# Optimization experiments

Hardware: AMD Instinct MI355X
Metric: run time of the kernel (lower is better)

## Reference

```python
import jax, jax.numpy as jnp
import numpy as np

NEG_SLOPE = 0.2  # PyG GATConv default leaky_relu slope
EPS = 1e-16


def setup_inputs() -> dict:
    key = jax.random.key(0)
    ks = jax.random.split(key, 8)
    N, E, F = 50000, 1600000, 128
    L, H, C = 3, 4, 32  # layers, heads, per-head channels; H*C == F
    Dh = 32             # MLP hidden (== hidden_channels)
    x = jax.random.normal(ks[0], (N, F), jnp.float32)
    edge_index = jax.random.randint(ks[1], (2, E), 0, N, jnp.int32)
    W = jax.random.normal(ks[2], (L, F, H * C), jnp.float32) * 0.1
    att_src = jax.random.normal(ks[3], (L, H, C), jnp.float32) * 0.1
    att_dst = jax.random.normal(ks[4], (L, H, C), jnp.float32) * 0.1
    b_conv = jnp.zeros((L, H * C), jnp.float32)
    W1 = jax.random.normal(ks[5], (F + H * C, Dh), jnp.float32) * 0.1
    b1 = jnp.zeros((Dh,), jnp.float32)
    W2 = jax.random.normal(ks[6], (Dh, 1), jnp.float32) * 0.1
    b2 = jnp.zeros((1,), jnp.float32)
    return {"x": x, "edge_index": edge_index, "W": W, "att_src": att_src,
            "att_dst": att_dst, "b_conv": b_conv, "W1": W1, "b1": b1,
            "W2": W2, "b2": b2}


def _gat_layer(x, src, dst, W, a_s, a_d, b, N):
    H, C = a_s.shape
    h = (x @ W).reshape(N, H, C)                      # [N,H,C]
    alpha_s = jnp.sum(h * a_s, axis=-1)               # [N,H]
    alpha_d = jnp.sum(h * a_d, axis=-1)               # [N,H]
    e = jax.nn.leaky_relu(alpha_s[src] + alpha_d[dst], NEG_SLOPE)  # [E,H]
    # segment softmax over incoming edges of each dst node
    m = jax.ops.segment_max(e, dst, num_segments=N)
    ex = jnp.exp(e - m[dst])
    s = jax.ops.segment_sum(ex, dst, num_segments=N)
    a = ex / (s[dst] + EPS)                           # [E,H]
    out = jax.ops.segment_sum(h[src] * a[:, :, None], dst, num_segments=N)
    return out.reshape(N, H * C) + b


def reference(x, edge_index, W, att_src, att_dst, b_conv, W1, b1, W2, b2):
    N = x.shape[0]
    loops = jnp.arange(N, dtype=edge_index.dtype)
    src = jnp.concatenate([edge_index[0], loops])  # PyG GATConv adds self loops
    dst = jnp.concatenate([edge_index[1], loops])
    x0 = x
    for l in range(W.shape[0]):
        x = _gat_layer(x, src, dst, W[l], att_src[l], att_dst[l], b_conv[l], N)
    h = jnp.concatenate([x, x0], axis=-1)
    h = jax.nn.relu(h @ W1 + b1)
    return jax.nn.sigmoid(h @ W2 + b2)
```

## Files before the change

### kernel.cpp

```cpp
#include <hip/hip_runtime.h>

#define NEG_SLOPE 0.2f
#define EPSF 1e-16f

typedef unsigned int uint;
typedef unsigned short ushort;
typedef __attribute__((ext_vector_type(8))) short short8;
typedef __attribute__((ext_vector_type(4))) float floatx4;

static __device__ __forceinline__ ushort f2bf(float f) {
    uint u = __float_as_uint(f);
    return (ushort)((u + 0x7FFFu + ((u >> 16) & 1u)) >> 16);
}
static __device__ __forceinline__ uint pack2(float a, float b) {
    return (uint)f2bf(a) | ((uint)f2bf(b) << 16);
}
static __device__ __forceinline__ float bf_lo(uint p) { return __uint_as_float(p << 16); }
static __device__ __forceinline__ float bf_hi(uint p) { return __uint_as_float(p & 0xFFFF0000u); }
static __device__ __forceinline__ short8 u2s8(uint4 v) {
    union { uint4 u; short8 s; } c; c.u = v; return c.s;
}
static __device__ __forceinline__ void load_lds16(const void* g, void* l) {
    __builtin_amdgcn_global_load_lds(
        (const __attribute__((address_space(1))) void*)g,
        (__attribute__((address_space(3))) void*)l, 16, 0, 0);
}

__global__ __launch_bounds__(256) void prep_kernel(
    const float* __restrict__ W, const float* __restrict__ W1,
    const float* __restrict__ x, uint4* __restrict__ Wp,
    uint4* __restrict__ W1p, uint4* __restrict__ xb,
    int* __restrict__ bucket_count, int L, int N)
{
    int id = blockIdx.x * 256 + threadIdx.x;
    const int nW = L * 2048;
    const int nX = N * 16;
    if (id < nW) {
        int l = id >> 11, s = id & 2047;
        int chunk = s >> 7, col = s & 127;
        const float* wp = W + (size_t)l * 16384 + (chunk * 8) * 128 + col;
        uint4 pk;
        pk.x = pack2(wp[0],   wp[128]);
        pk.y = pack2(wp[256], wp[384]);
        pk.z = pack2(wp[512], wp[640]);
        pk.w = pack2(wp[768], wp[896]);
        Wp[id] = pk;
    } else if (id < nW + 1024) {
        int s = id - nW;
        int chunk = s >> 5, col = s & 31;
        const float* wp = W1 + (chunk * 8) * 32 + col;
        uint4 pk;
        pk.x = pack2(wp[0],   wp[32]);
        pk.y = pack2(wp[64],  wp[96]);
        pk.z = pack2(wp[128], wp[160]);
        pk.w = pack2(wp[192], wp[224]);
        W1p[s] = pk;
    } else if (id < nW + 1024 + nX) {
        int xid = id - nW - 1024;
        int row = xid >> 4, c8 = xid & 15;
        const float4* xp = (const float4*)(x + (size_t)row * 128 + c8 * 8);
        float4 v0 = xp[0], v1 = xp[1];
        uint4 pk;
        pk.x = pack2(v0.x, v0.y); pk.y = pack2(v0.z, v0.w);
        pk.z = pack2(v1.x, v1.y); pk.w = pack2(v1.z, v1.w);
        xb[xid] = pk;
    } else if (id < nW + 1024 + nX + 256) {
        bucket_count[id - nW - 1024 - nX] = 0;
    }
}

#define GA_LDS_BYTES ((2048 + 1040) * 16)
__global__ __launch_bounds__(256) void gemm_alpha_kernel(
    const uint4* __restrict__ xb, const uint4* __restrict__ Wp,
    const float* __restrict__ att_s, const float* __restrict__ att_d,
    uint* __restrict__ h2, float* __restrict__ alpha_s,
    float* __restrict__ alpha_d, int N)
{
    __shared__ __align__(16) char smraw[GA_LDS_BYTES];
    uint4* sW = (uint4*)smraw;
    uint4* sX = sW + 2048;
    float* sD = (float*)smraw;

    const int t = threadIdx.x;
    const int wb = t & ~63;
    const int rowBase = blockIdx.x * 64;

#pragma unroll
    for (int i = 0; i < 8; ++i)
        load_lds16(Wp + i * 256 + t, sW + i * 256 + wb);

#pragma unroll
    for (int i = 0; i < 4; ++i) {
        int f = t + i * 256;
        int row = f >> 4, c8 = f & 15;
        uint4 v = make_uint4(0u, 0u, 0u, 0u);
        if (rowBase + row < N) v = xb[(size_t)(rowBase + row) * 16 + c8];
        sX[c8 * 65 + row] = v;
    }
    __syncthreads();

    const int w = t >> 6, lane = t & 63, q = lane >> 4, l15 = lane & 15;
    short8 a[4];
#pragma unroll
    for (int s = 0; s < 4; ++s)
        a[s] = u2s8(sX[(4 * s + q) * 65 + 16 * w + l15]);

    floatx4 acc[8];
#pragma unroll
    for (int ct = 0; ct < 8; ++ct) acc[ct] = (floatx4){0.f, 0.f, 0.f, 0.f};
#pragma unroll
    for (int ct = 0; ct < 8; ++ct) {
#pragma unroll
        for (int s = 0; s < 4; ++s) {
            short8 b = u2s8(sW[(4 * s + q) * 128 + 16 * ct + l15]);
            acc[ct] = __builtin_amdgcn_mfma_f32_16x16x32_bf16(a[s], b, acc[ct], 0, 0, 0);
        }
    }
    __syncthreads();

#pragma unroll
    for (int ct = 0; ct < 8; ++ct) {
#pragma unroll
        for (int r = 0; r < 4; ++r)
            sD[(16 * w + 4 * q + r) * 129 + 16 * ct + l15] = acc[ct][r];
    }
    __syncthreads();

#pragma unroll
    for (int i = 0; i < 4; ++i) {
        int slot = t + i * 256;
        int row = slot >> 4, c8 = slot & 15;
        if (rowBase + row < N) {
            const float* dp = &sD[row * 129 + c8 * 8];
            uint4 o;
            o.x = pack2(dp[0], dp[1]); o.y = pack2(dp[2], dp[3]);
            o.z = pack2(dp[4], dp[5]); o.w = pack2(dp[6], dp[7]);
            ((uint4*)h2)[(size_t)(rowBase + row) * 16 + c8] = o;
        }
    }
    {
        int row = t & 63, head = t >> 6;
        if (rowBase + row < N) {
            const float* dp = &sD[row * 129 + head * 32];
            const float* asp = att_s + head * 32;
            const float* adp = att_d + head * 32;
            float ps = 0.f, pd = 0.f;
#pragma unroll
            for (int c = 0; c < 32; ++c) { float v = dp[c]; ps += v * asp[c]; pd += v * adp[c]; }
            alpha_s[(size_t)(rowBase + row) * 4 + head] = ps;
            alpha_d[(size_t)(rowBase + row) * 4 + head] = pd;
        }
    }
}

__global__ __launch_bounds__(256) void bucket_count_kernel(
    const int* __restrict__ ei, int E, int NB, int* __restrict__ bucket_count)
{
    __shared__ int cnt[256];
    cnt[threadIdx.x] = 0;
    __syncthreads();
    const int base = blockIdx.x * 2048 + threadIdx.x;
#pragma unroll
    for (int j = 0; j < 8; ++j) {
        int idx = base + j * 256;
        if (idx < E) atomicAdd(&cnt[ei[E + idx] >> 8], 1);
    }
    __syncthreads();
    int c = cnt[threadIdx.x];
    if (threadIdx.x < NB && c) atomicAdd(&bucket_count[threadIdx.x], c);
}

__global__ __launch_bounds__(256) void bucket_scan_kernel(
    const int* __restrict__ bucket_count, int NB,
    int* __restrict__ bucket_base, int* __restrict__ bucket_cursor,
    int* __restrict__ row_start, int N)
{
    __shared__ int s[256];
    const int t = threadIdx.x;
    int v = (t < NB) ? bucket_count[t] : 0;
    s[t] = v;
    __syncthreads();
    for (int off = 1; off < 256; off <<= 1) {
        int x = s[t];
        int a = (t >= off) ? s[t - off] : 0;
        __syncthreads();
        s[t] = x + a;
        __syncthreads();
    }
    int ex = s[t] - v;
    if (t < NB) { bucket_base[t] = ex; bucket_cursor[t] = ex; }
    if (t == 255) { bucket_base[NB] = s[255]; row_start[N] = s[255]; }
}

__global__ __launch_bounds__(256) void distribute_kernel(
    const int* __restrict__ ei, int E, int NB,
    int* __restrict__ bucket_cursor, uint* __restrict__ bdata)
{
    __shared__ int cnt[256];
    __shared__ int bbase[256];
    cnt[threadIdx.x] = 0;
    __syncthreads();
    const int base = blockIdx.x * 2048 + threadIdx.x;
    int srcs[8], dsts[8], rank[8];
#pragma unroll
    for (int j = 0; j < 8; ++j) {
        int idx = base + j * 256;
        if (idx < E) {
            srcs[j] = ei[idx];
            dsts[j] = ei[E + idx];
            rank[j] = atomicAdd(&cnt[dsts[j] >> 8], 1);
        } else dsts[j] = -1;
    }
    __syncthreads();
    {
        int c = cnt[threadIdx.x];
        bbase[threadIdx.x] = (threadIdx.x < NB && c) ? atomicAdd(&bucket_cursor[threadIdx.x], c) : 0;
    }
    __syncthreads();
#pragma unroll
    for (int j = 0; j < 8; ++j) {
        if (dsts[j] >= 0) {
            int b = dsts[j] >> 8;
            bdata[bbase[b] + rank[j]] = (uint)srcs[j] | ((uint)(dsts[j] & 255) << 16);
        }
    }
}

#define BCAP 12800
__global__ __launch_bounds__(256) void bucket_csr_kernel(
    const uint* __restrict__ bdata, const int* __restrict__ bucket_base,
    int* __restrict__ row_start, ushort* __restrict__ csr_src, int N)
{
    __shared__ int hist[256];
    __shared__ int scn[256];
    __shared__ int cur[256];
    __shared__ ushort buf[BCAP];
    const int b = blockIdx.x;
    const int t = threadIdx.x;
    const int beg = bucket_base[b];
    const int sz = bucket_base[b + 1] - beg;
    hist[t] = 0;
    __syncthreads();
    for (int i = t; i < sz; i += 256) atomicAdd(&hist[bdata[beg + i] >> 16], 1);
    __syncthreads();
    int v = hist[t];
    scn[t] = v;
    __syncthreads();
    for (int off = 1; off < 256; off <<= 1) {
        int x = scn[t];
        int a = (t >= off) ? scn[t - off] : 0;
        __syncthreads();
        scn[t] = x + a;
        __syncthreads();
    }
    int ex = scn[t] - v;
    cur[t] = ex;
    int node = b * 256 + t;
    if (node < N) row_start[node] = beg + ex;
    __syncthreads();
    if (sz <= BCAP) {
        for (int i = t; i < sz; i += 256) {
            uint d = bdata[beg + i];
            int pos = atomicAdd(&cur[d >> 16], 1);
            buf[pos] = (ushort)(d & 0xFFFFu);
        }
        __syncthreads();
        for (int i = t; i < sz; i += 256) csr_src[beg + i] = buf[i];
    } else {
        for (int i = t; i < sz; i += 256) {
            uint d = bdata[beg + i];
            int pos = atomicAdd(&cur[d >> 16], 1);
            csr_src[beg + pos] = (ushort)(d & 0xFFFFu);
        }
    }
}

__global__ __launch_bounds__(256) void agg_csr_kernel(
    const ushort* __restrict__ csr_src, const int* __restrict__ row_start,
    const float* __restrict__ alpha_s, const float* __restrict__ alpha_d,
    const uint* __restrict__ h2, const float* __restrict__ b,
    uint4* __restrict__ outb, int N)
{
    const int g = (blockIdx.x * 256 + threadIdx.x) >> 4;
    const int l = threadIdx.x & 15;
    if (g >= N) return;
    const int head = l >> 2;
    const uint4* h4 = (const uint4*)h2;

    const float ad = alpha_d[g * 4 + head];

    float e = alpha_s[g * 4 + head] + ad;
    e = e > 0.f ? e : NEG_SLOPE * e;
    float ex = __expf(e);
    uint4 q = h4[(size_t)g * 16 + l];
    float a0 = ex * bf_lo(q.x), a1 = ex * bf_hi(q.x);
    float a2 = ex * bf_lo(q.y), a3 = ex * bf_hi(q.y);
    float a4 = ex * bf_lo(q.z), a5 = ex * bf_hi(q.z);
    float a6 = ex * bf_lo(q.w), a7 = ex * bf_hi(q.w);
    float sx = ex;

    const int beg = row_start[g];
    const int end = row_start[g + 1];
    int k = beg;
    for (; k + 4 <= end; k += 4) {
        int s0 = csr_src[k], s1 = csr_src[k + 1];
        int s2 = csr_src[k + 2], s3 = csr_src[k + 3];
        uint4 q0 = h4[(size_t)s0 * 16 + l];
        uint4 q1 = h4[(size_t)s1 * 16 + l];
        uint4 q2 = h4[(size_t)s2 * 16 + l];
        uint4 q3 = h4[(size_t)s3 * 16 + l];
        float e0 = alpha_s[s0 * 4 + head] + ad;
        float e1 = alpha_s[s1 * 4 + head] + ad;
        float e2 = alpha_s[s2 * 4 + head] + ad;
        float e3 = alpha_s[s3 * 4 + head] + ad;
        e0 = e0 > 0.f ? e0 : NEG_SLOPE * e0;
        e1 = e1 > 0.f ? e1 : NEG_SLOPE * e1;
        e2 = e2 > 0.f ? e2 : NEG_SLOPE * e2;
        e3 = e3 > 0.f ? e3 : NEG_SLOPE * e3;
        float x0 = __expf(e0), x1 = __expf(e1);
        float x2 = __expf(e2), x3 = __expf(e3);
        a0 += x0 * bf_lo(q0.x) + x1 * bf_lo(q1.x) + x2 * bf_lo(q2.x) + x3 * bf_lo(q3.x);
        a1 += x0 * bf_hi(q0.x) + x1 * bf_hi(q1.x) + x2 * bf_hi(q2.x) + x3 * bf_hi(q3.x);
        a2 += x0 * bf_lo(q0.y) + x1 * bf_lo(q1.y) + x2 * bf_lo(q2.y) + x3 * bf_lo(q3.y);
        a3 += x0 * bf_hi(q0.y) + x1 * bf_hi(q1.y) + x2 * bf_hi(q2.y) + x3 * bf_hi(q3.y);
        a4 += x0 * bf_lo(q0.z) + x1 * bf_lo(q1.z) + x2 * bf_lo(q2.z) + x3 * bf_lo(q3.z);
        a5 += x0 * bf_hi(q0.z) + x1 * bf_hi(q1.z) + x2 * bf_hi(q2.z) + x3 * bf_hi(q3.z);
        a6 += x0 * bf_lo(q0.w) + x1 * bf_lo(q1.w) + x2 * bf_lo(q2.w) + x3 * bf_lo(q3.w);
        a7 += x0 * bf_hi(q0.w) + x1 * bf_hi(q1.w) + x2 * bf_hi(q2.w) + x3 * bf_hi(q3.w);
        sx += x0 + x1 + x2 + x3;
    }
    for (; k < end; ++k) {
        int s0 = csr_src[k];
        float e0 = alpha_s[s0 * 4 + head] + ad;
        uint4 q0 = h4[(size_t)s0 * 16 + l];
        e0 = e0 > 0.f ? e0 : NEG_SLOPE * e0;
        float x0 = __expf(e0);
        a0 += x0 * bf_lo(q0.x); a1 += x0 * bf_hi(q0.x);
        a2 += x0 * bf_lo(q0.y); a3 += x0 * bf_hi(q0.y);
        a4 += x0 * bf_lo(q0.z); a5 += x0 * bf_hi(q0.z);
        a6 += x0 * bf_lo(q0.w); a7 += x0 * bf_hi(q0.w);
        sx += x0;
    }
    const float inv = 1.f / (sx + EPSF);
    const float4 b0 = ((const float4*)b)[l * 2];
    const float4 b1 = ((const float4*)b)[l * 2 + 1];
    uint4 o;
    o.x = pack2(b0.x + a0 * inv, b0.y + a1 * inv);
    o.y = pack2(b0.z + a2 * inv, b0.w + a3 * inv);
    o.z = pack2(b1.x + a4 * inv, b1.y + a5 * inv);
    o.w = pack2(b1.z + a6 * inv, b1.w + a7 * inv);
    outb[(size_t)g * 16 + l] = o;
}

__global__ __launch_bounds__(256) void mlp_kernel(
    const uint4* __restrict__ xb3, const uint4* __restrict__ xb0,
    const uint4* __restrict__ W1p, const float* __restrict__ b1,
    const float* __restrict__ W2, const float* __restrict__ b2,
    float* __restrict__ out, int N)
{
    __shared__ __align__(16) uint4 sA[32 * 65];
    __shared__ __align__(16) uint4 sB[32 * 32];
    const int t = threadIdx.x;
    const int wb = t & ~63;
    const int rowBase = blockIdx.x * 64;

#pragma unroll
    for (int i = 0; i < 4; ++i)
        load_lds16(W1p + i * 256 + t, sB + i * 256 + wb);
#pragma unroll
    for (int i = 0; i < 8; ++i) {
        int f = t + i * 256;
        int c = f & 31, row = f >> 5;
        uint4 v = make_uint4(0u, 0u, 0u, 0u);
        int grow = rowBase + row;
        if (grow < N)
            v = (c < 16) ? xb3[(size_t)grow * 16 + c]
                         : xb0[(size_t)grow * 16 + (c - 16)];
        sA[c * 65 + row] = v;
    }
    __syncthreads();

    const int w = t >> 6, lane = t & 63, q = lane >> 4, l15 = lane & 15;
    floatx4 acc0 = (floatx4){0.f, 0.f, 0.f, 0.f};
    floatx4 acc1 = (floatx4){0.f, 0.f, 0.f, 0.f};
#pragma unroll
    for (int s = 0; s < 8; ++s) {
        short8 a = u2s8(sA[(4 * s + q) * 65 + 16 * w + l15]);
        acc0 = __builtin_amdgcn_mfma_f32_16x16x32_bf16(a, u2s8(sB[(4 * s + q) * 32 + l15]), acc0, 0, 0, 0);
        acc1 = __builtin_amdgcn_mfma_f32_16x16x32_bf16(a, u2s8(sB[(4 * s + q) * 32 + 16 + l15]), acc1, 0, 0, 0);
    }
    const float b1a = b1[l15], b1b = b1[16 + l15];
    const float w2a = W2[l15], w2b = W2[16 + l15];
    const float b2v = b2[0];
#pragma unroll
    for (int r = 0; r < 4; ++r) {
        int row = rowBase + 16 * w + 4 * q + r;
        float v0 = acc0[r] + b1a; v0 = v0 > 0.f ? v0 : 0.f;
        float v1 = acc1[r] + b1b; v1 = v1 > 0.f ? v1 : 0.f;
        float p = v0 * w2a + v1 * w2b;
        p += __shfl_xor(p, 1);
        p += __shfl_xor(p, 2);
        p += __shfl_xor(p, 4);
        p += __shfl_xor(p, 8);
        if (l15 == 0 && row < N)
            out[row] = 1.f / (1.f + __expf(-(p + b2v)));
    }
}

extern "C" void kernel_launch(void* const* d_in, const int* in_sizes, int n_in,
                              void* d_out, int out_size, void* d_ws, size_t ws_size,
                              hipStream_t stream)
{
    const float* x       = (const float*)d_in[0];
    const int*   ei      = (const int*)d_in[1];
    const float* W       = (const float*)d_in[2];
    const float* att_src = (const float*)d_in[3];
    const float* att_dst = (const float*)d_in[4];
    const float* b_conv  = (const float*)d_in[5];
    const float* W1      = (const float*)d_in[6];
    const float* b1      = (const float*)d_in[7];
    const float* W2      = (const float*)d_in[8];
    const float* b2      = (const float*)d_in[9];
    float* outp = (float*)d_out;

    const int N = in_sizes[0] / 128;
    const int E = in_sizes[1] / 2;
    const int L = in_sizes[2] / (128 * 128);
    const int NB = (N + 255) >> 8;

    char* ws = (char*)d_ws;
    uint*  h2      = (uint*)ws;
    uint4* xb0     = (uint4*)(h2 + (size_t)N * 64);
    uint4* xb      = xb0 + (size_t)N * 16;
    float* alpha_s = (float*)(xb + (size_t)N * 16);
    float* alpha_d = alpha_s + (size_t)N * 4;
    uint4* Wp      = (uint4*)(alpha_d + (size_t)N * 4);
    uint4* W1p     = Wp + (size_t)L * 2048;
    int* bucket_count  = (int*)(W1p + 1024);
    int* bucket_base   = bucket_count + 256;
    int* bucket_cursor = bucket_base + 260;
    int* row_start     = bucket_cursor + 256;
    uint* bdata        = (uint*)(row_start + N + 1);
    ushort* csr_src    = (ushort*)(bdata + E);

    const int nbE = (E + 2047) / 2048;
    const int prepItems = L * 2048 + 1024 + N * 16 + 256;

    prep_kernel<<<(prepItems + 255) / 256, 256, 0, stream>>>(
        W, W1, x, Wp, W1p, xb0, bucket_count, L, N);

    bucket_count_kernel<<<nbE, 256, 0, stream>>>(ei, E, NB, bucket_count);
    bucket_scan_kernel<<<1, 256, 0, stream>>>(bucket_count, NB, bucket_base,
                                              bucket_cursor, row_start, N);
    distribute_kernel<<<nbE, 256, 0, stream>>>(ei, E, NB, bucket_cursor, bdata);
    bucket_csr_kernel<<<NB, 256, 0, stream>>>(bdata, bucket_base, row_start,
                                              csr_src, N);

    for (int l = 0; l < L; ++l) {
        const uint4* xin = (l == 0) ? xb0 : xb;
        const uint4* Wl  = Wp + (size_t)l * 2048;
        const float* asl = att_src + (size_t)l * 128;
        const float* adl = att_dst + (size_t)l * 128;
        const float* bl  = b_conv + (size_t)l * 128;

        gemm_alpha_kernel<<<(N + 63) / 64, 256, 0, stream>>>(
            xin, Wl, asl, adl, h2, alpha_s, alpha_d, N);

        agg_csr_kernel<<<(N * 16 + 255) / 256, 256, 0, stream>>>(
            csr_src, row_start, alpha_s, alpha_d, h2, bl, xb, N);
    }

    mlp_kernel<<<(N + 63) / 64, 256, 0, stream>>>(
        xb, xb0, W1p, b1, W2, b2, outp, N);
}
```

Baseline: 387.7 us.

## Sort CSR neighbors by source segment, fuse prep with bucket count, nontemporal agg stores

The CSR build now sub-sorts each destination's incoming edges by the high bits of the source index (8 segments), so the gather in the aggregation kernel visits source rows in a more localized order and should reuse cache better. The separate bucket-count kernel is merged into the prep kernel as extra blocks, with the counter zeroed by a memset, which removes one launch. Aggregation output is written with nontemporal stores to avoid polluting cache. The CSR kernel uses larger LDS histograms (2048 bins), which may lower occupancy.

```diff
diff --git a/kernel.cpp b/kernel.cpp
--- a/kernel.cpp
+++ b/kernel.cpp
@@ -2,11 +2,13 @@
 
 #define NEG_SLOPE 0.2f
 #define EPSF 1e-16f
+#define SEG_SHIFT 13
 
 typedef unsigned int uint;
 typedef unsigned short ushort;
 typedef __attribute__((ext_vector_type(8))) short short8;
 typedef __attribute__((ext_vector_type(4))) float floatx4;
+typedef __attribute__((ext_vector_type(4))) uint uintx4;
 
 static __device__ __forceinline__ ushort f2bf(float f) {
     uint u = __float_as_uint(f);
@@ -26,12 +28,28 @@
         (__attribute__((address_space(3))) void*)l, 16, 0, 0);
 }
 
-__global__ __launch_bounds__(256) void prep_kernel(
+__global__ __launch_bounds__(256) void prep_count_kernel(
     const float* __restrict__ W, const float* __restrict__ W1,
     const float* __restrict__ x, uint4* __restrict__ Wp,
     uint4* __restrict__ W1p, uint4* __restrict__ xb,
-    int* __restrict__ bucket_count, int L, int N)
-{
+    const int* __restrict__ ei, int E, int NB,
+    int* __restrict__ bucket_count, int L, int N, int nbPrep)
+{
+    __shared__ int cnt[256];
+    if ((int)blockIdx.x >= nbPrep) {
+        cnt[threadIdx.x] = 0;
+        __syncthreads();
+        const int base = (blockIdx.x - nbPrep) * 2048 + threadIdx.x;
+#pragma unroll
+        for (int j = 0; j < 8; ++j) {
+            int idx = base + j * 256;
+            if (idx < E) atomicAdd(&cnt[ei[E + idx] >> 8], 1);
+        }
+        __syncthreads();
+        int c = cnt[threadIdx.x];
+        if ((int)threadIdx.x < NB && c) atomicAdd(&bucket_count[threadIdx.x], c);
+        return;
+    }
     int id = blockIdx.x * 256 + threadIdx.x;
     const int nW = L * 2048;
     const int nX = N * 16;
@@ -64,8 +82,6 @@
         pk.x = pack2(v0.x, v0.y); pk.y = pack2(v0.z, v0.w);
         pk.z = pack2(v1.x, v1.y); pk.w = pack2(v1.z, v1.w);
         xb[xid] = pk;
-    } else if (id < nW + 1024 + nX + 256) {
-        bucket_count[id - nW - 1024 - nX] = 0;
     }
 }
 
@@ -153,23 +169,6 @@
     }
 }
 
-__global__ __launch_bounds__(256) void bucket_count_kernel(
-    const int* __restrict__ ei, int E, int NB, int* __restrict__ bucket_count)
-{
-    __shared__ int cnt[256];
-    cnt[threadIdx.x] = 0;
-    __syncthreads();
-    const int base = blockIdx.x * 2048 + threadIdx.x;
-#pragma unroll
-    for (int j = 0; j < 8; ++j) {
-        int idx = base + j * 256;
-        if (idx < E) atomicAdd(&cnt[ei[E + idx] >> 8], 1);
-    }
-    __syncthreads();
-    int c = cnt[threadIdx.x];
-    if (threadIdx.x < NB && c) atomicAdd(&bucket_count[threadIdx.x], c);
-}
-
 __global__ __launch_bounds__(256) void bucket_scan_kernel(
     const int* __restrict__ bucket_count, int NB,
     int* __restrict__ bucket_base, int* __restrict__ bucket_cursor,
@@ -214,7 +213,7 @@
     __syncthreads();
     {
         int c = cnt[threadIdx.x];
-        bbase[threadIdx.x] = (threadIdx.x < NB && c) ? atomicAdd(&bucket_cursor[threadIdx.x], c) : 0;
+        bbase[threadIdx.x] = ((int)threadIdx.x < NB && c) ? atomicAdd(&bucket_cursor[threadIdx.x], c) : 0;
     }
     __syncthreads();
 #pragma unroll
@@ -231,20 +230,27 @@
     const uint* __restrict__ bdata, const int* __restrict__ bucket_base,
     int* __restrict__ row_start, ushort* __restrict__ csr_src, int N)
 {
-    __shared__ int hist[256];
+    __shared__ int hist[2048];
+    __shared__ int cur[2048];
     __shared__ int scn[256];
-    __shared__ int cur[256];
     __shared__ ushort buf[BCAP];
     const int b = blockIdx.x;
     const int t = threadIdx.x;
     const int beg = bucket_base[b];
     const int sz = bucket_base[b + 1] - beg;
-    hist[t] = 0;
-    __syncthreads();
-    for (int i = t; i < sz; i += 256) atomicAdd(&hist[bdata[beg + i] >> 16], 1);
-    __syncthreads();
-    int v = hist[t];
-    scn[t] = v;
+#pragma unroll
+    for (int j = 0; j < 8; ++j) hist[t * 8 + j] = 0;
+    __syncthreads();
+    for (int i = t; i < sz; i += 256) {
+        uint d = bdata[beg + i];
+        int key = (int)((d >> 16) << 3) | (int)((d & 0xFFFFu) >> SEG_SHIFT);
+        atomicAdd(&hist[key], 1);
+    }
+    __syncthreads();
+    int local[8]; int s = 0;
+#pragma unroll
+    for (int j = 0; j < 8; ++j) { local[j] = hist[t * 8 + j]; s += local[j]; }
+    scn[t] = s;
     __syncthreads();
     for (int off = 1; off < 256; off <<= 1) {
         int x = scn[t];
@@ -253,15 +259,18 @@
         scn[t] = x + a;
         __syncthreads();
     }
-    int ex = scn[t] - v;
-    cur[t] = ex;
+    int run = scn[t] - s;
+#pragma unroll
+    for (int j = 0; j < 8; ++j) { cur[t * 8 + j] = run; run += local[j]; }
+    __syncthreads();
     int node = b * 256 + t;
-    if (node < N) row_start[node] = beg + ex;
+    if (node < N) row_start[node] = beg + cur[t << 3];
     __syncthreads();
     if (sz <= BCAP) {
         for (int i = t; i < sz; i += 256) {
             uint d = bdata[beg + i];
-            int pos = atomicAdd(&cur[d >> 16], 1);
+            int key = (int)((d >> 16) << 3) | (int)((d & 0xFFFFu) >> SEG_SHIFT);
+            int pos = atomicAdd(&cur[key], 1);
             buf[pos] = (ushort)(d & 0xFFFFu);
         }
         __syncthreads();
@@ -269,7 +278,8 @@
     } else {
         for (int i = t; i < sz; i += 256) {
             uint d = bdata[beg + i];
-            int pos = atomicAdd(&cur[d >> 16], 1);
+            int key = (int)((d >> 16) << 3) | (int)((d & 0xFFFFu) >> SEG_SHIFT);
+            int pos = atomicAdd(&cur[key], 1);
             csr_src[beg + pos] = (ushort)(d & 0xFFFFu);
         }
     }
@@ -279,7 +289,7 @@
     const ushort* __restrict__ csr_src, const int* __restrict__ row_start,
     const float* __restrict__ alpha_s, const float* __restrict__ alpha_d,
     const uint* __restrict__ h2, const float* __restrict__ b,
-    uint4* __restrict__ outb, int N)
+    uint* __restrict__ outb, int N)
 {
     const int g = (blockIdx.x * 256 + threadIdx.x) >> 4;
     const int l = threadIdx.x & 15;
@@ -344,12 +354,12 @@
     const float inv = 1.f / (sx + EPSF);
     const float4 b0 = ((const float4*)b)[l * 2];
     const float4 b1 = ((const float4*)b)[l * 2 + 1];
-    uint4 o;
+    uintx4 o;
     o.x = pack2(b0.x + a0 * inv, b0.y + a1 * inv);
     o.y = pack2(b0.z + a2 * inv, b0.w + a3 * inv);
     o.z = pack2(b1.x + a4 * inv, b1.y + a5 * inv);
     o.w = pack2(b1.z + a6 * inv, b1.w + a7 * inv);
-    outb[(size_t)g * 16 + l] = o;
+    __builtin_nontemporal_store(o, (uintx4*)(outb + (size_t)g * 64 + l * 4));
 }
 
 __global__ __launch_bounds__(256) void mlp_kernel(
@@ -444,12 +454,14 @@
     ushort* csr_src    = (ushort*)(bdata + E);
 
     const int nbE = (E + 2047) / 2048;
-    const int prepItems = L * 2048 + 1024 + N * 16 + 256;
-
-    prep_kernel<<<(prepItems + 255) / 256, 256, 0, stream>>>(
-        W, W1, x, Wp, W1p, xb0, bucket_count, L, N);
-
-    bucket_count_kernel<<<nbE, 256, 0, stream>>>(ei, E, NB, bucket_count);
+    const int prepItems = L * 2048 + 1024 + N * 16;
+    const int nbPrep = (prepItems + 255) / 256;
+
+    (void)hipMemsetAsync(bucket_count, 0, 256 * sizeof(int), stream);
+
+    prep_count_kernel<<<nbPrep + nbE, 256, 0, stream>>>(
+        W, W1, x, Wp, W1p, xb0, ei, E, NB, bucket_count, L, N, nbPrep);
+
     bucket_scan_kernel<<<1, 256, 0, stream>>>(bucket_count, NB, bucket_base,
                                               bucket_cursor, row_start, N);
     distribute_kernel<<<nbE, 256, 0, stream>>>(ei, E, NB, bucket_cursor, bdata);
@@ -467,7 +479,7 @@
             xin, Wl, asl, adl, h2, alpha_s, alpha_d, N);
 
         agg_csr_kernel<<<(N * 16 + 255) / 256, 256, 0, stream>>>(
-            csr_src, row_start, alpha_s, alpha_d, h2, bl, xb, N);
+            csr_src, row_start, alpha_s, alpha_d, h2, bl, (uint*)xb, N);
     }
 
     mlp_kernel<<<(N + 63) / 64, 256, 0, stream>>>(
```

Result: faster. 359.8 us (-7.2%).
